# Kernel optimization log

Hardware: AMD Instinct MI355X
Metric: run time of the kernel (lower is better)

Reference implementation:

```python
import jax, jax.numpy as jnp
import numpy as np

N = 50000      # nodes
E = 800000     # edges (before self-loops)
F_IN = 768     # num_features
H = 128        # hidden_dim
C = 9          # num_classes
M = 3          # num_mid_layers
BN_EPS = 1e-5

def _glorot(k, shape):
    lim = float(np.sqrt(6.0 / (shape[-2] + shape[-1])))
    return jax.random.uniform(k, shape, jnp.float32, -lim, lim)

def setup_inputs() -> dict:
    key = jax.random.key(0)
    ks = jax.random.split(key, 24)
    x = jax.random.normal(ks[0], (N, F_IN), jnp.float32)
    edge_index = jax.random.randint(ks[1], (2, E), 0, N)
    edge_type = jax.random.randint(ks[2], (E,), 0, 5)
    edge_distance = jax.random.uniform(ks[3], (E,), jnp.float32)
    # GATConv params (heads=1): W [in,out], att_src/att_dst [out], bias [out]
    W0 = _glorot(ks[4], (F_IN, H)); a0s = _glorot(ks[5], (1, H))[0]; a0d = _glorot(ks[6], (1, H))[0]; b0 = jnp.zeros((H,), jnp.float32)
    Wm = _glorot(ks[7], (M, H, H)); ams = _glorot(ks[8], (M, 1, H))[:, 0]; amd = _glorot(ks[9], (M, 1, H))[:, 0]; bm = jnp.zeros((M, H), jnp.float32)
    W4 = _glorot(ks[10], (H, C)); a4s = _glorot(ks[11], (1, C))[0]; a4d = _glorot(ks[12], (1, C))[0]; b4 = jnp.zeros((C,), jnp.float32)
    # BatchNorm params for the M+1 norms actually used in forward (all dim H)
    gamma = jnp.ones((M + 1, H), jnp.float32)
    beta = jnp.zeros((M + 1, H), jnp.float32)
    return {"x": x, "edge_index": edge_index, "edge_type": edge_type, "edge_distance": edge_distance,
            "W0": W0, "a0s": a0s, "a0d": a0d, "b0": b0,
            "Wm": Wm, "ams": ams, "amd": amd, "bm": bm,
            "W4": W4, "a4s": a4s, "a4d": a4d, "b4": b4,
            "gamma": gamma, "beta": beta}

def _leaky(x, s):
    return jnp.where(x >= 0, x, s * x)

def _gat_conv(x, src, dst, W, a_s, a_d, b):
    # x: [N, in] -> h: [N, out]; attention per edge j->i, softmax over incoming edges of i
    h = x @ W
    alpha_src = h @ a_s            # [N]
    alpha_dst = h @ a_d            # [N]
    e = _leaky(alpha_src[src] + alpha_dst[dst], 0.2)   # [Etot]
    m = jax.ops.segment_max(e, dst, num_segments=N)
    ex = jnp.exp(e - m[dst])
    z = jax.ops.segment_sum(ex, dst, num_segments=N)
    alpha = ex / z[dst]
    out = jax.ops.segment_sum(h[src] * alpha[:, None], dst, num_segments=N)
    return out + b

def _bn_train(x, g, be):
    mu = x.mean(0)
    var = x.var(0)   # biased, as BatchNorm1d uses for normalization
    return (x - mu) * jax.lax.rsqrt(var + BN_EPS) * g + be

def reference(x, edge_index, edge_type, edge_distance,
              W0, a0s, a0d, b0, Wm, ams, amd, bm, W4, a4s, a4d, b4, gamma, beta):
    loops = jnp.arange(N, dtype=edge_index.dtype)
    src = jnp.concatenate([edge_index[0], loops])   # add self-loops (PyG default)
    dst = jnp.concatenate([edge_index[1], loops])
    h = _gat_conv(x, src, dst, W0, a0s, a0d, b0)
    for i in range(M):
        t = _leaky(_bn_train(h, gamma[i], beta[i]), 0.1)
        h = _gat_conv(t, src, dst, Wm[i], ams[i], amd[i], bm[i]) + t
    h = _leaky(_bn_train(h, gamma[M], beta[M]), 0.1)
    h = _gat_conv(h, src, dst, W4, a4s, a4d, b4)
    return _leaky(h, 0.1)
```

## Files before the change

kernel.cpp:

```cpp
#include <hip/hip_runtime.h>
#include <hip/hip_bf16.h>

#define N_NODES 50000
#define N_EDGES 800000
#define F_INN   768
#define HID     128
#define N_CLS   9
#define ETOT    (N_EDGES + N_NODES)
#define BN_EPS  1e-5f
#define INV_N   (1.0f / (float)N_NODES)

typedef __hip_bfloat16 bf16;
typedef __attribute__((ext_vector_type(8))) short bf16x8;
typedef __attribute__((ext_vector_type(4))) float f32x4;

__device__ __forceinline__ float leaky(float v, float s) { return v >= 0.0f ? v : s * v; }
__device__ __forceinline__ int clampn(int s) {
  return ((unsigned)s < (unsigned)N_NODES) ? s : 0;
}
__device__ __forceinline__ short f2bs(float f) {
  bf16 h = __float2bfloat16(f);
  return __builtin_bit_cast(short, h);
}
__device__ __forceinline__ float bs2f(unsigned short u) {
  unsigned v = ((unsigned)u) << 16;
  return __builtin_bit_cast(float, v);
}
__device__ __forceinline__ void gload_lds16(const void* g, void* l) {
  __builtin_amdgcn_global_load_lds((const __attribute__((address_space(1))) void*)g,
                                   (__attribute__((address_space(3))) void*)l, 16, 0, 0);
}

__global__ void k_pack(const float* __restrict__ W0, const float* __restrict__ Wm,
                       short* __restrict__ W0T, short* __restrict__ WmT) {
  int i = blockIdx.x * blockDim.x + threadIdx.x;
  if (i < F_INN * HID) {
    int n = i / F_INN, k = i % F_INN;
    W0T[i] = f2bs(W0[k * HID + n]);
  } else if (i < F_INN * HID + 3 * HID * HID) {
    int j = i - F_INN * HID;
    int l = j / (HID * HID), rem = j % (HID * HID);
    int n = rem / HID, k = rem % HID;
    WmT[j] = f2bs(Wm[(l * HID + k) * HID + n]);
  }
}

__global__ void k_init_deg(int* fill) {
  int i = blockIdx.x * blockDim.x + threadIdx.x;
  if (i < N_NODES) fill[i] = 1;
}

__global__ void k_count(const int* __restrict__ dst, int* fill) {
  int e = blockIdx.x * blockDim.x + threadIdx.x;
  if (e < N_EDGES) atomicAdd(&fill[clampn(dst[e])], 1);
}

__global__ void k_scan(int* fill, int* row_ptr) {
  __shared__ int wsum[16], wpre[16];
  int tid = threadIdx.x, lane = tid & 63, wv = tid >> 6;
  int carry = 0;
  for (int base = 0; base < N_NODES; base += 1024) {
    int i = base + tid;
    int v = (i < N_NODES) ? fill[i] : 0;
    if (i < N_NODES) fill[i] = 0;
    int sc = v;
#pragma unroll
    for (int off = 1; off < 64; off <<= 1) {
      int t = __shfl_up(sc, off);
      if (lane >= off) sc += t;
    }
    if (lane == 63) wsum[wv] = sc;
    __syncthreads();
    if (tid < 16) {
      int s = wsum[tid];
#pragma unroll
      for (int off = 1; off < 16; off <<= 1) {
        int t = __shfl_up(s, off);
        if (tid >= off) s += t;
      }
      wpre[tid] = s;
    }
    __syncthreads();
    int woff = wv ? wpre[wv - 1] : 0;
    if (i < N_NODES) row_ptr[i] = carry + woff + sc - v;
    carry += wpre[15];
    __syncthreads();
  }
  if (tid == 0) row_ptr[N_NODES] = carry;
}

__global__ void k_place(const int* __restrict__ src, const int* __restrict__ dst,
                        const int* __restrict__ row_ptr, int* fill, int* csr_src) {
  int id = blockIdx.x * blockDim.x + threadIdx.x;
  if (id >= ETOT) return;
  int s, d;
  if (id < N_EDGES) { s = clampn(src[id]); d = clampn(dst[id]); }
  else { s = id - N_EDGES; d = s; }
  int p = atomicAdd(&fill[d], 1);
  csr_src[row_ptr[d] + p] = s;
}

template <int K, bool BN>
__global__ __launch_bounds__(512, 5)
void k_gemm_mfma(const float* __restrict__ X, const short* __restrict__ BT,
                 const float* __restrict__ stats, const float* __restrict__ gamma,
                 const float* __restrict__ beta,
                 const float* __restrict__ a_s, const float* __restrict__ a_d,
                 short* __restrict__ hb, float* __restrict__ asrc,
                 float* __restrict__ adst) {
  constexpr int NS = K / 32;
  constexpr int SPC = 4;
  constexpr int CH = NS / SPC;
  constexpr int ROWB = K * 4;
  constexpr int XB = 16 * ROWB;
  __shared__ float4 xs4[XB / 16];
  __shared__ float psA[8][16], psD[8][16];
  __shared__ float scs[HID], sfs[HID];
  char* xs = (char*)xs4;

  int tid = threadIdx.x;
  int wid = tid >> 6, lane = tid & 63;
  int m = lane & 15, q = lane >> 4;
  int row0 = blockIdx.x * 16;
  int col0 = wid * 16;

  const short* bbase = BT + (size_t)(col0 + m) * K + q * 8;
  f32x4 acc = (f32x4){0.f, 0.f, 0.f, 0.f};
  bf16x8 bb0[SPC], bb1[SPC];

  auto loadC = [&](bf16x8* dst, int c) {
#pragma unroll
    for (int i = 0; i < SPC; ++i)
      dst[i] = *(const bf16x8*)(bbase + (size_t)(c * SPC + i) * 32);
  };
  auto computeC = [&](const bf16x8* bw, int c) {
#pragma unroll
    for (int i = 0; i < SPC; ++i) {
      int s = c * SPC + i;
      int kb = s * 128 + q * 32;
      int sw = (m & 7) << 4;
      float4 x0 = *(const float4*)(xs + m * ROWB + (kb ^ sw));
      float4 x1 = *(const float4*)(xs + m * ROWB + ((kb + 16) ^ sw));
      float xv[8] = {x0.x, x0.y, x0.z, x0.w, x1.x, x1.y, x1.z, x1.w};
      if (BN) {
        int k0 = s * 32 + q * 8;
#pragma unroll
        for (int j = 0; j < 8; ++j) xv[j] = leaky(xv[j] * scs[k0 + j] + sfs[k0 + j], 0.1f);
      }
      bf16x8 a;
#pragma unroll
      for (int j = 0; j < 8; ++j) a[j] = f2bs(xv[j]);
      acc = __builtin_amdgcn_mfma_f32_16x16x32_bf16(a, bw[i], acc, 0, 0, 0);
    }
  };

  if (BN && tid < HID) {
    float mu = stats[tid] * INV_N;
    float var = fmaxf(stats[HID + tid] * INV_N - mu * mu, 0.0f);
    float rs = rsqrtf(var + BN_EPS);
    float g = gamma[tid];
    scs[tid] = g * rs;
    sfs[tid] = beta[tid] - mu * g * rs;
  }

  loadC(bb0, 0);
  if (CH > 1) loadC(bb1, 1);
  asm volatile("" ::: "memory");
  constexpr int ROUNDS = XB / 8192;
#pragma unroll
  for (int r = 0; r < ROUNDS; ++r) {
    int o = r * 8192 + tid * 16;
    int row = o / ROWB;
    int bb = o - row * ROWB;
    int sw = (row & 7) << 4;
    gload_lds16((const char*)X + (size_t)(row0 + row) * ROWB + (bb ^ sw), xs + o);
  }
  __syncthreads();

#pragma unroll
  for (int c = 0; c < CH; ++c) {
    if (c & 1) {
      computeC(bb1, c);
      if (c + 2 < CH) { loadC(bb1, c + 2); asm volatile("" ::: "memory"); }
    } else {
      computeC(bb0, c);
      if (c + 2 < CH) { loadC(bb0, c + 2); asm volatile("" ::: "memory"); }
    }
  }

  float av = a_s[col0 + m], dv = a_d[col0 + m];
  float sr[4], dr[4];
#pragma unroll
  for (int r = 0; r < 4; ++r) {
    float cc = acc[r];
    hb[(size_t)(row0 + q * 4 + r) * HID + col0 + m] = f2bs(cc);
    sr[r] = cc * av;
    dr[r] = cc * dv;
  }
#pragma unroll
  for (int r = 0; r < 4; ++r) {
#pragma unroll
    for (int off = 1; off < 16; off <<= 1) {
      sr[r] += __shfl_xor(sr[r], off);
      dr[r] += __shfl_xor(dr[r], off);
    }
  }
  if (m == 0) {
#pragma unroll
    for (int r = 0; r < 4; ++r) {
      psA[wid][q * 4 + r] = sr[r];
      psD[wid][q * 4 + r] = dr[r];
    }
  }
  __syncthreads();
  if (tid < 16) {
    float s = 0.f, d = 0.f;
#pragma unroll
    for (int w2 = 0; w2 < 8; ++w2) { s += psA[w2][tid]; d += psD[w2][tid]; }
    asrc[row0 + tid] = s;
    adst[row0 + tid] = d;
  }
}

__device__ __forceinline__ void acc8(float* a, float e, uint4 v) {
  a[0] += e * bs2f((unsigned short)(v.x & 0xffffu));
  a[1] += e * bs2f((unsigned short)(v.x >> 16));
  a[2] += e * bs2f((unsigned short)(v.y & 0xffffu));
  a[3] += e * bs2f((unsigned short)(v.y >> 16));
  a[4] += e * bs2f((unsigned short)(v.z & 0xffffu));
  a[5] += e * bs2f((unsigned short)(v.z >> 16));
  a[6] += e * bs2f((unsigned short)(v.w & 0xffffu));
  a[7] += e * bs2f((unsigned short)(v.w >> 16));
}

__global__ void k_agg128(const unsigned short* __restrict__ h, const float* __restrict__ asrc,
                         const float* __restrict__ adst, const int* __restrict__ row_ptr,
                         const int* __restrict__ csr_src, const float* __restrict__ bias,
                         const float* __restrict__ hres, const float* __restrict__ stats,
                         const float* __restrict__ gamma, const float* __restrict__ beta,
                         float* __restrict__ out, float* __restrict__ zeroP) {
  __shared__ int   lds_ss[4][64];
  __shared__ float lds_ex[4][64];
  if (zeroP && blockIdx.x == 0 && threadIdx.x < 256) zeroP[threadIdx.x] = 0.0f;
  int wid = (blockIdx.x * blockDim.x + threadIdx.x) >> 6;
  int lane = threadIdx.x & 63;
  int w = (threadIdx.x >> 6) & 3;
  if (wid >= N_NODES) return;
  int beg = row_ptr[wid], end = row_ptr[wid + 1];
  int cnt0 = end - beg;
  float adsti = adst[wid];
  int g = lane & 15, es = lane >> 4;
  float z = 0.f;
  float a[8];
#pragma unroll
  for (int k = 0; k < 8; ++k) a[k] = 0.f;

  if (cnt0 <= 64) {
    int sl = 0;
    float v = -1e30f;
    if (lane < cnt0) {
      sl = clampn(csr_src[beg + lane]);
      v = leaky(asrc[sl] + adsti, 0.2f);
    }
    float mx = v;
#pragma unroll
    for (int off = 1; off < 64; off <<= 1) mx = fmaxf(mx, __shfl_xor(mx, off));
    float ex = (lane < cnt0) ? __expf(v - mx) : 0.f;
    lds_ss[w][lane] = sl;
    lds_ex[w][lane] = ex;
    __builtin_amdgcn_wave_barrier();
    float zs = 0.f;
    for (int jb = 0; jb < cnt0; jb += 8) {
      int j0 = jb + es, j1 = jb + 4 + es;
      int s0 = lds_ss[w][j0]; float e0 = lds_ex[w][j0];
      int s1 = lds_ss[w][j1]; float e1 = lds_ex[w][j1];
      uint4 v0 = *(const uint4*)(h + (size_t)s0 * HID + g * 8);
      uint4 v1 = *(const uint4*)(h + (size_t)s1 * HID + g * 8);
      zs += e0 + e1;
      acc8(a, e0, v0);
      acc8(a, e1, v1);
    }
    z = zs;
  } else {
    float mx = -1e30f;
    for (int cb = beg; cb < end; cb += 64) {
      int e = cb + lane;
      if (e < end) {
        int s = clampn(csr_src[e]);
        mx = fmaxf(mx, leaky(asrc[s] + adsti, 0.2f));
      }
    }
#pragma unroll
    for (int off = 1; off < 64; off <<= 1) mx = fmaxf(mx, __shfl_xor(mx, off));
    float zs = 0.f;
    for (int cb = beg; cb < end; cb += 64) {
      int cnt = min(64, end - cb);
      int sl = 0;
      float ex = 0.f;
      if (lane < cnt) {
        sl = clampn(csr_src[cb + lane]);
        ex = __expf(leaky(asrc[sl] + adsti, 0.2f) - mx);
      }
      lds_ss[w][lane] = sl;
      lds_ex[w][lane] = ex;
      __builtin_amdgcn_wave_barrier();
      for (int jb = 0; jb < cnt; jb += 8) {
        int j0 = jb + es, j1 = jb + 4 + es;
        int s0 = lds_ss[w][j0]; float e0 = lds_ex[w][j0];
        int s1 = lds_ss[w][j1]; float e1 = lds_ex[w][j1];
        uint4 v0 = *(const uint4*)(h + (size_t)s0 * HID + g * 8);
        uint4 v1 = *(const uint4*)(h + (size_t)s1 * HID + g * 8);
        zs += e0 + e1;
        acc8(a, e0, v0);
        acc8(a, e1, v1);
      }
      __builtin_amdgcn_wave_barrier();
    }
    z = zs;
  }
#pragma unroll
  for (int k = 0; k < 8; ++k) {
    a[k] += __shfl_xor(a[k], 16);
    a[k] += __shfl_xor(a[k], 32);
  }
  z += __shfl_xor(z, 16);
  z += __shfl_xor(z, 32);
  float inv = (z > 0.0f) ? 1.0f / z : 0.0f;
  if (lane < 16) {
    int c0 = g * 8;
    float o[8];
#pragma unroll
    for (int k = 0; k < 8; ++k) o[k] = a[k] * inv + bias[c0 + k];
    if (hres) {
      float hr[8];
      *(float4*)(hr)     = *(const float4*)(hres + (size_t)wid * HID + c0);
      *(float4*)(hr + 4) = *(const float4*)(hres + (size_t)wid * HID + c0 + 4);
#pragma unroll
      for (int k = 0; k < 8; ++k) {
        int c = c0 + k;
        float mu = stats[c] * INV_N;
        float var = fmaxf(stats[HID + c] * INV_N - mu * mu, 0.0f);
        float rs = rsqrtf(var + BN_EPS);
        float sc = gamma[c] * rs;
        float sf = beta[c] - mu * sc;
        o[k] += leaky(hr[k] * sc + sf, 0.1f);
      }
    }
    *(float4*)(out + (size_t)wid * HID + c0)     = *(float4*)(o);
    *(float4*)(out + (size_t)wid * HID + c0 + 4) = *(float4*)(o + 4);
  }
}

__global__ void k_bn_stats(const float* __restrict__ h, float* stats) {
  int f = threadIdx.x;
  int r0 = blockIdx.x * 128;
  int r1 = min(r0 + 128, N_NODES);
  float s = 0.0f, s2 = 0.0f;
#pragma unroll 8
  for (int r = r0; r < r1; ++r) {
    float v = h[(size_t)r * HID + f];
    s += v;
    s2 += v * v;
  }
  atomicAdd(&stats[f], s);
  atomicAdd(&stats[HID + f], s2);
}

__global__ void k_final_gemm(const float* __restrict__ h, const float* __restrict__ stats,
                             const float* __restrict__ gamma, const float* __restrict__ beta,
                             const float* __restrict__ W4,
                             const float* __restrict__ a4s, const float* __restrict__ a4d,
                             float* __restrict__ h4, float* __restrict__ asrc,
                             float* __restrict__ adst) {
  int row = (blockIdx.x * blockDim.x + threadIdx.x) >> 6;
  int lane = threadIdx.x & 63;
  if (row >= N_NODES) return;
  int c1 = lane + 64;
  float mu0 = stats[lane] * INV_N;
  float va0 = fmaxf(stats[HID + lane] * INV_N - mu0 * mu0, 0.0f);
  float rs0 = rsqrtf(va0 + BN_EPS);
  float sc0 = gamma[lane] * rs0, sf0 = beta[lane] - mu0 * sc0;
  float mu1 = stats[c1] * INV_N;
  float va1 = fmaxf(stats[HID + c1] * INV_N - mu1 * mu1, 0.0f);
  float rs1 = rsqrtf(va1 + BN_EPS);
  float sc1 = gamma[c1] * rs1, sf1 = beta[c1] - mu1 * sc1;
  float t0 = leaky(h[(size_t)row * HID + lane] * sc0 + sf0, 0.1f);
  float t1 = leaky(h[(size_t)row * HID + c1] * sc1 + sf1, 0.1f);
  float myv = 0.0f, s = 0.0f, d = 0.0f;
#pragma unroll
  for (int c = 0; c < N_CLS; ++c) {
    float p = t0 * W4[lane * N_CLS + c] + t1 * W4[(lane + 64) * N_CLS + c];
#pragma unroll
    for (int m = 32; m; m >>= 1) p += __shfl_xor(p, m);
    s += p * a4s[c];
    d += p * a4d[c];
    if (lane == c) myv = p;
  }
  if (lane < N_CLS) h4[(size_t)row * N_CLS + lane] = myv;
  if (lane == 0) { asrc[row] = s; adst[row] = d; }
}

__global__ void k_final_agg(const float* __restrict__ h4, const float* __restrict__ asrc,
                            const float* __restrict__ adst, const int* __restrict__ row_ptr,
                            const int* __restrict__ csr_src, const float* __restrict__ b4,
                            float* __restrict__ out) {
  __shared__ int   lds_ss[4][64];
  __shared__ float lds_ex[4][64];
  int wid = (blockIdx.x * blockDim.x + threadIdx.x) >> 6;
  int lane = threadIdx.x & 63;
  int w = (threadIdx.x >> 6) & 3;
  if (wid >= N_NODES) return;
  int beg = row_ptr[wid], end = row_ptr[wid + 1];
  int cnt0 = end - beg;
  float adsti = adst[wid];
  int g = lane & 15, es = lane >> 4;
  float zs = 0.f, av = 0.f;
  if (cnt0 <= 64) {
    int sl = 0;
    float v = -1e30f;
    if (lane < cnt0) {
      sl = clampn(csr_src[beg + lane]);
      v = leaky(asrc[sl] + adsti, 0.2f);
    }
    float mx = v;
#pragma unroll
    for (int off = 1; off < 64; off <<= 1) mx = fmaxf(mx, __shfl_xor(mx, off));
    float ex = (lane < cnt0) ? __expf(v - mx) : 0.f;
    lds_ss[w][lane] = sl;
    lds_ex[w][lane] = ex;
    __builtin_amdgcn_wave_barrier();
    for (int jb = 0; jb < cnt0; jb += 4) {
      int j = jb + es;
      int s = lds_ss[w][j];
      float e = lds_ex[w][j];
      zs += e;
      if (g < N_CLS) av += e * h4[(size_t)s * N_CLS + g];
    }
  } else {
    float mx = -1e30f;
    for (int cb = beg; cb < end; cb += 64) {
      int e = cb + lane;
      if (e < end) {
        int s = clampn(csr_src[e]);
        mx = fmaxf(mx, leaky(asrc[s] + adsti, 0.2f));
      }
    }
#pragma unroll
    for (int off = 1; off < 64; off <<= 1) mx = fmaxf(mx, __shfl_xor(mx, off));
    for (int cb = beg; cb < end; cb += 64) {
      int cnt = min(64, end - cb);
      int sl = 0;
      float ex = 0.f;
      if (lane < cnt) {
        sl = clampn(csr_src[cb + lane]);
        ex = __expf(leaky(asrc[sl] + adsti, 0.2f) - mx);
      }
      lds_ss[w][lane] = sl;
      lds_ex[w][lane] = ex;
      __builtin_amdgcn_wave_barrier();
      for (int jb = 0; jb < cnt; jb += 4) {
        int j = jb + es;
        int s = lds_ss[w][j];
        float e = lds_ex[w][j];
        zs += e;
        if (g < N_CLS) av += e * h4[(size_t)s * N_CLS + g];
      }
      __builtin_amdgcn_wave_barrier();
    }
  }
  float z = zs;
  z += __shfl_xor(z, 16); z += __shfl_xor(z, 32);
  av += __shfl_xor(av, 16); av += __shfl_xor(av, 32);
  if (lane < N_CLS) {
    float o = (z > 0.0f) ? av / z : 0.0f;
    o = leaky(o + b4[lane], 0.1f);
    out[(size_t)wid * N_CLS + lane] = o;
  }
}

extern "C" void kernel_launch(void* const* d_in, const int* in_sizes, int n_in,
                              void* d_out, int out_size, void* d_ws, size_t ws_size,
                              hipStream_t stream) {
  const float* x   = (const float*)d_in[0];
  const int*   ei  = (const int*)d_in[1];
  const int*   src = ei;
  const int*   dst = ei + N_EDGES;
  const float* W0  = (const float*)d_in[4];
  const float* a0s = (const float*)d_in[5];
  const float* a0d = (const float*)d_in[6];
  const float* b0  = (const float*)d_in[7];
  const float* Wm  = (const float*)d_in[8];
  const float* ams = (const float*)d_in[9];
  const float* amd = (const float*)d_in[10];
  const float* bm  = (const float*)d_in[11];
  const float* W4  = (const float*)d_in[12];
  const float* a4s = (const float*)d_in[13];
  const float* a4d = (const float*)d_in[14];
  const float* b4  = (const float*)d_in[15];
  const float* gam = (const float*)d_in[16];
  const float* bet = (const float*)d_in[17];
  float* out = (float*)d_out;

  int* row_ptr   = (int*)d_ws;
  int* fill      = row_ptr + 50004;
  int* csr_src   = fill + N_NODES;
  short* W0T     = (short*)(csr_src + ETOT);
  short* WmT     = W0T + F_INN * HID;
  short* bufA    = WmT + 3 * HID * HID;
  float* asrc    = (float*)(bufA + (size_t)N_NODES * HID);
  float* adst    = asrc + N_NODES;
  float* pstat   = adst + N_NODES;
  float* h4      = pstat + 512;
  float* bufB    = h4 + (size_t)N_NODES * N_CLS;
  float* PST[2]  = {pstat, pstat + 256};

  const int B256 = 256;
  int gN    = (N_NODES + B256 - 1) / B256;
  int gE    = (N_EDGES + B256 - 1) / B256;
  int gET   = (ETOT + B256 - 1) / B256;
  int gWav  = (N_NODES + 3) / 4;
  int gMfma = N_NODES / 16;
  int gBN   = (N_NODES + 127) / 128;
  int gPack = (F_INN * HID + 3 * HID * HID + B256 - 1) / B256;

  k_pack<<<gPack, B256, 0, stream>>>(W0, Wm, W0T, WmT);
  k_init_deg<<<gN, B256, 0, stream>>>(fill);
  k_count<<<gE, B256, 0, stream>>>(dst, fill);
  k_scan<<<1, 1024, 0, stream>>>(fill, row_ptr);
  k_place<<<gET, B256, 0, stream>>>(src, dst, row_ptr, fill, csr_src);

  k_gemm_mfma<F_INN, false><<<gMfma, 512, 0, stream>>>(x, W0T, nullptr, nullptr, nullptr,
                                                       a0s, a0d, bufA, asrc, adst);
  k_agg128<<<gWav, B256, 0, stream>>>((const unsigned short*)bufA, asrc, adst, row_ptr,
                                      csr_src, b0, nullptr, nullptr, nullptr, nullptr,
                                      bufB, PST[0]);

  for (int i = 0; i < 3; ++i) {
    k_bn_stats<<<gBN, HID, 0, stream>>>(bufB, PST[i & 1]);
    k_gemm_mfma<HID, true><<<gMfma, 512, 0, stream>>>(bufB, WmT + i * HID * HID,
                                                      PST[i & 1], gam + i * HID, bet + i * HID,
                                                      ams + i * HID, amd + i * HID,
                                                      bufA, asrc, adst);
    k_agg128<<<gWav, B256, 0, stream>>>((const unsigned short*)bufA, asrc, adst, row_ptr,
                                        csr_src, bm + i * HID, bufB, PST[i & 1],
                                        gam + i * HID, bet + i * HID, bufB, PST[(i + 1) & 1]);
  }

  k_bn_stats<<<gBN, HID, 0, stream>>>(bufB, PST[1]);
  k_final_gemm<<<gWav, B256, 0, stream>>>(bufB, PST[1], gam + 3 * HID, bet + 3 * HID,
                                          W4, a4s, a4d, h4, asrc, adst);
  k_final_agg<<<gWav, B256, 0, stream>>>(h4, asrc, adst, row_ptr, csr_src, b4, out);
}
```

Measured before the change: 808.0 us.

## Make MFMA GEMM persistent with register-resident weights and double-buffered LDS staging

Measured after the change: 775.4 us. -4.0%, faster.

```diff
diff --git a/kernel.cpp b/kernel.cpp
--- a/kernel.cpp
+++ b/kernel.cpp
@@ -9,6 +9,7 @@
 #define ETOT    (N_EDGES + N_NODES)
 #define BN_EPS  1e-5f
 #define INV_N   (1.0f / (float)N_NODES)
+#define NT16    (N_NODES / 16)
 
 typedef __hip_bfloat16 bf16;
 typedef __attribute__((ext_vector_type(8))) short bf16x8;
@@ -29,6 +30,14 @@
 __device__ __forceinline__ void gload_lds16(const void* g, void* l) {
   __builtin_amdgcn_global_load_lds((const __attribute__((address_space(1))) void*)g,
                                    (__attribute__((address_space(3))) void*)l, 16, 0, 0);
+}
+__device__ __forceinline__ void blk_barrier() {
+  asm volatile("" ::: "memory");
+  __builtin_amdgcn_s_barrier();
+  __builtin_amdgcn_sched_barrier(0);
+}
+__device__ __forceinline__ void lgkm0() {
+  asm volatile("s_waitcnt lgkmcnt(0)" ::: "memory");
 }
 
 __global__ void k_pack(const float* __restrict__ W0, const float* __restrict__ Wm,
@@ -101,124 +110,148 @@
 }
 
 template <int K, bool BN>
-__global__ __launch_bounds__(512, 5)
+__global__ __launch_bounds__(512, 2)
 void k_gemm_mfma(const float* __restrict__ X, const short* __restrict__ BT,
                  const float* __restrict__ stats, const float* __restrict__ gamma,
                  const float* __restrict__ beta,
                  const float* __restrict__ a_s, const float* __restrict__ a_d,
                  short* __restrict__ hb, float* __restrict__ asrc,
                  float* __restrict__ adst) {
-  constexpr int NS = K / 32;
-  constexpr int SPC = 4;
-  constexpr int CH = NS / SPC;
-  constexpr int ROWB = K * 4;
-  constexpr int XB = 16 * ROWB;
-  __shared__ float4 xs4[XB / 16];
+  constexpr int KSUB  = (K > 384) ? 384 : K;
+  constexpr int NSUB  = K / KSUB;
+  constexpr int NS    = KSUB / 32;
+  constexpr int LPT   = KSUB / 128;
+  constexpr int NSLOT = KSUB * 2;
+  __shared__ float4 bufF[2][KSUB * 4];
+  __shared__ bf16x8 bufH[NSLOT];
+  __shared__ float scs[HID], sfs[HID];
   __shared__ float psA[8][16], psD[8][16];
-  __shared__ float scs[HID], sfs[HID];
-  char* xs = (char*)xs4;
-
-  int tid = threadIdx.x;
-  int wid = tid >> 6, lane = tid & 63;
-  int m = lane & 15, q = lane >> 4;
-  int row0 = blockIdx.x * 16;
-  int col0 = wid * 16;
-
-  const short* bbase = BT + (size_t)(col0 + m) * K + q * 8;
-  f32x4 acc = (f32x4){0.f, 0.f, 0.f, 0.f};
-  bf16x8 bb0[SPC], bb1[SPC];
-
-  auto loadC = [&](bf16x8* dst, int c) {
-#pragma unroll
-    for (int i = 0; i < SPC; ++i)
-      dst[i] = *(const bf16x8*)(bbase + (size_t)(c * SPC + i) * 32);
-  };
-  auto computeC = [&](const bf16x8* bw, int c) {
-#pragma unroll
-    for (int i = 0; i < SPC; ++i) {
-      int s = c * SPC + i;
-      int kb = s * 128 + q * 32;
-      int sw = (m & 7) << 4;
-      float4 x0 = *(const float4*)(xs + m * ROWB + (kb ^ sw));
-      float4 x1 = *(const float4*)(xs + m * ROWB + ((kb + 16) ^ sw));
-      float xv[8] = {x0.x, x0.y, x0.z, x0.w, x1.x, x1.y, x1.z, x1.w};
-      if (BN) {
-        int k0 = s * 32 + q * 8;
-#pragma unroll
-        for (int j = 0; j < 8; ++j) xv[j] = leaky(xv[j] * scs[k0 + j] + sfs[k0 + j], 0.1f);
-      }
-      bf16x8 a;
-#pragma unroll
-      for (int j = 0; j < 8; ++j) a[j] = f2bs(xv[j]);
-      acc = __builtin_amdgcn_mfma_f32_16x16x32_bf16(a, bw[i], acc, 0, 0, 0);
-    }
-  };
+
+  const int tid = threadIdx.x;
+  const int wv = tid >> 6, lane = tid & 63;
+  const int m = lane & 15, q = lane >> 4;
+  const int col = wv * 16 + m;
+  const int bid = blockIdx.x;
+  const int nrt = (NT16 - bid + 255) >> 8;
+  const int T = nrt * NSUB;
+
+  bf16x8 breg[K / 32];
+  {
+    const short* bb = BT + (size_t)col * K + q * 8;
+#pragma unroll
+    for (int c = 0; c < K / 32; ++c) breg[c] = *(const bf16x8*)(bb + c * 32);
+  }
+  const float av = a_s[col], dv = a_d[col];
 
   if (BN && tid < HID) {
     float mu = stats[tid] * INV_N;
     float var = fmaxf(stats[HID + tid] * INV_N - mu * mu, 0.0f);
     float rs = rsqrtf(var + BN_EPS);
-    float g = gamma[tid];
-    scs[tid] = g * rs;
-    sfs[tid] = beta[tid] - mu * g * rs;
-  }
-
-  loadC(bb0, 0);
-  if (CH > 1) loadC(bb1, 1);
-  asm volatile("" ::: "memory");
-  constexpr int ROUNDS = XB / 8192;
-#pragma unroll
-  for (int r = 0; r < ROUNDS; ++r) {
-    int o = r * 8192 + tid * 16;
-    int row = o / ROWB;
-    int bb = o - row * ROWB;
-    int sw = (row & 7) << 4;
-    gload_lds16((const char*)X + (size_t)(row0 + row) * ROWB + (bb ^ sw), xs + o);
-  }
-  __syncthreads();
-
-#pragma unroll
-  for (int c = 0; c < CH; ++c) {
-    if (c & 1) {
-      computeC(bb1, c);
-      if (c + 2 < CH) { loadC(bb1, c + 2); asm volatile("" ::: "memory"); }
+    float g2 = gamma[tid];
+    scs[tid] = g2 * rs;
+    sfs[tid] = beta[tid] - mu * g2 * rs;
+  }
+
+  auto STAGE = [&](int t) {
+    int r0 = (bid + (t / NSUB) * 256) * 16;
+    int kb = (NSUB == 2) ? (t & 1) * KSUB : 0;
+    int buf = t & 1;
+#pragma unroll
+    for (int r = 0; r < LPT; ++r) {
+      int d = r * 512 + tid;
+      int row = d & 15, c = d >> 4;
+      gload_lds16(X + (size_t)(r0 + row) * K + kb + c * 4, &bufF[buf][d]);
+    }
+  };
+
+  STAGE(0);
+  if (T > 1) STAGE(1);
+  lgkm0();
+  blk_barrier();
+
+  f32x4 acc = (f32x4){0.f, 0.f, 0.f, 0.f};
+  for (int t = 0; t < T; ++t) {
+    const int ks = (NSUB == 2) ? (t & 1) : 0;
+    const int buf = t & 1;
+    if (t + 1 < T) {
+      if constexpr (LPT == 3) asm volatile("s_waitcnt vmcnt(3)" ::: "memory");
+      else                    asm volatile("s_waitcnt vmcnt(1)" ::: "memory");
     } else {
-      computeC(bb0, c);
-      if (c + 2 < CH) { loadC(bb0, c + 2); asm volatile("" ::: "memory"); }
-    }
-  }
-
-  float av = a_s[col0 + m], dv = a_d[col0 + m];
-  float sr[4], dr[4];
-#pragma unroll
-  for (int r = 0; r < 4; ++r) {
-    float cc = acc[r];
-    hb[(size_t)(row0 + q * 4 + r) * HID + col0 + m] = f2bs(cc);
-    sr[r] = cc * av;
-    dr[r] = cc * dv;
-  }
-#pragma unroll
-  for (int r = 0; r < 4; ++r) {
-#pragma unroll
-    for (int off = 1; off < 16; off <<= 1) {
-      sr[r] += __shfl_xor(sr[r], off);
-      dr[r] += __shfl_xor(dr[r], off);
-    }
-  }
-  if (m == 0) {
-#pragma unroll
-    for (int r = 0; r < 4; ++r) {
-      psA[wid][q * 4 + r] = sr[r];
-      psD[wid][q * 4 + r] = dr[r];
-    }
-  }
-  __syncthreads();
-  if (tid < 16) {
-    float s = 0.f, d = 0.f;
-#pragma unroll
-    for (int w2 = 0; w2 < 8; ++w2) { s += psA[w2][tid]; d += psD[w2][tid]; }
-    asrc[row0 + tid] = s;
-    adst[row0 + tid] = d;
+      asm volatile("s_waitcnt vmcnt(0)" ::: "memory");
+    }
+    blk_barrier();
+#pragma unroll
+    for (int j = 0; j < (NSLOT + 511) / 512; ++j) {
+      int sl = j * 512 + tid;
+      if (sl < NSLOT) {
+        int s = sl >> 6, lp = sl & 63;
+        int mp = lp & 15, qp = lp >> 4;
+        int k0 = s * 32 + qp * 8;
+        int d = (k0 >> 2) * 16 + mp;
+        float4 x0 = bufF[buf][d];
+        float4 x1 = bufF[buf][d + 16];
+        float xv[8] = {x0.x, x0.y, x0.z, x0.w, x1.x, x1.y, x1.z, x1.w};
+        if (BN) {
+#pragma unroll
+          for (int jj = 0; jj < 8; ++jj)
+            xv[jj] = leaky(xv[jj] * scs[k0 + jj] + sfs[k0 + jj], 0.1f);
+        }
+        bf16x8 hv;
+#pragma unroll
+        for (int jj = 0; jj < 8; ++jj) hv[jj] = f2bs(xv[jj]);
+        bufH[sl] = hv;
+      }
+    }
+    lgkm0();
+    blk_barrier();
+    if (t + 2 < T) STAGE(t + 2);
+    if (NSUB == 2 && ks == 1) {
+#pragma unroll
+      for (int s = 0; s < NS; ++s)
+        acc = __builtin_amdgcn_mfma_f32_16x16x32_bf16(bufH[s * 64 + lane],
+                                                      breg[NS + s], acc, 0, 0, 0);
+    } else {
+#pragma unroll
+      for (int s = 0; s < NS; ++s)
+        acc = __builtin_amdgcn_mfma_f32_16x16x32_bf16(bufH[s * 64 + lane],
+                                                      breg[s], acc, 0, 0, 0);
+    }
+    if (ks == NSUB - 1) {
+      int r0 = (bid + (t / NSUB) * 256) * 16;
+      float sr[4], dr[4];
+#pragma unroll
+      for (int r = 0; r < 4; ++r) {
+        float cc = acc[r];
+        hb[(size_t)(r0 + q * 4 + r) * HID + col] = f2bs(cc);
+        sr[r] = cc * av;
+        dr[r] = cc * dv;
+      }
+      acc = (f32x4){0.f, 0.f, 0.f, 0.f};
+#pragma unroll
+      for (int r = 0; r < 4; ++r) {
+#pragma unroll
+        for (int off = 1; off < 16; off <<= 1) {
+          sr[r] += __shfl_xor(sr[r], off);
+          dr[r] += __shfl_xor(dr[r], off);
+        }
+      }
+      if (m == 0) {
+#pragma unroll
+        for (int r = 0; r < 4; ++r) {
+          psA[wv][q * 4 + r] = sr[r];
+          psD[wv][q * 4 + r] = dr[r];
+        }
+      }
+      lgkm0();
+      blk_barrier();
+      if (tid < 16) {
+        float s2 = 0.f, d2 = 0.f;
+#pragma unroll
+        for (int w2 = 0; w2 < 8; ++w2) { s2 += psA[w2][tid]; d2 += psD[w2][tid]; }
+        asrc[r0 + tid] = s2;
+        adst[r0 + tid] = d2;
+      }
+    }
   }
 }
 
@@ -269,17 +302,26 @@
     lds_ss[w][lane] = sl;
     lds_ex[w][lane] = ex;
     __builtin_amdgcn_wave_barrier();
+    int nr = (cnt0 + 7) >> 3;
+    int s0 = lds_ss[w][es],     s1 = lds_ss[w][es + 4];
+    float e0 = lds_ex[w][es],   e1 = lds_ex[w][es + 4];
+    uint4 v0 = *(const uint4*)(h + (size_t)s0 * HID + g * 8);
+    uint4 v1 = *(const uint4*)(h + (size_t)s1 * HID + g * 8);
     float zs = 0.f;
-    for (int jb = 0; jb < cnt0; jb += 8) {
-      int j0 = jb + es, j1 = jb + 4 + es;
-      int s0 = lds_ss[w][j0]; float e0 = lds_ex[w][j0];
-      int s1 = lds_ss[w][j1]; float e1 = lds_ex[w][j1];
-      uint4 v0 = *(const uint4*)(h + (size_t)s0 * HID + g * 8);
-      uint4 v1 = *(const uint4*)(h + (size_t)s1 * HID + g * 8);
+    for (int r = 1; r < nr; ++r) {
+      int j0 = r * 8 + es, j1 = r * 8 + 4 + es;
+      int t0 = lds_ss[w][j0];   float f0 = lds_ex[w][j0];
+      int t1 = lds_ss[w][j1];   float f1 = lds_ex[w][j1];
+      uint4 n0 = *(const uint4*)(h + (size_t)t0 * HID + g * 8);
+      uint4 n1 = *(const uint4*)(h + (size_t)t1 * HID + g * 8);
       zs += e0 + e1;
       acc8(a, e0, v0);
       acc8(a, e1, v1);
-    }
+      v0 = n0; v1 = n1; e0 = f0; e1 = f1;
+    }
+    zs += e0 + e1;
+    acc8(a, e0, v0);
+    acc8(a, e1, v1);
     z = zs;
   } else {
     float mx = -1e30f;
@@ -429,13 +471,21 @@
     lds_ss[w][lane] = sl;
     lds_ex[w][lane] = ex;
     __builtin_amdgcn_wave_barrier();
-    for (int jb = 0; jb < cnt0; jb += 4) {
-      int j = jb + es;
-      int s = lds_ss[w][j];
-      float e = lds_ex[w][j];
-      zs += e;
-      if (g < N_CLS) av += e * h4[(size_t)s * N_CLS + g];
-    }
+    int nr = (cnt0 + 3) >> 2;
+    int s0 = lds_ss[w][es];
+    float e0 = lds_ex[w][es];
+    float hv0 = (g < N_CLS) ? h4[(size_t)s0 * N_CLS + g] : 0.f;
+    for (int r = 1; r < nr; ++r) {
+      int j = r * 4 + es;
+      int s1 = lds_ss[w][j];
+      float e1 = lds_ex[w][j];
+      float hv1 = (g < N_CLS) ? h4[(size_t)s1 * N_CLS + g] : 0.f;
+      zs += e0;
+      av += e0 * hv0;
+      s0 = s1; e0 = e1; hv0 = hv1;
+    }
+    zs += e0;
+    av += e0 * hv0;
   } else {
     float mx = -1e30f;
     for (int cb = beg; cb < end; cb += 64) {
@@ -519,7 +569,6 @@
   int gE    = (N_EDGES + B256 - 1) / B256;
   int gET   = (ETOT + B256 - 1) / B256;
   int gWav  = (N_NODES + 3) / 4;
-  int gMfma = N_NODES / 16;
   int gBN   = (N_NODES + 127) / 128;
   int gPack = (F_INN * HID + 3 * HID * HID + B256 - 1) / B256;
 
@@ -529,18 +578,18 @@
   k_scan<<<1, 1024, 0, stream>>>(fill, row_ptr);
   k_place<<<gET, B256, 0, stream>>>(src, dst, row_ptr, fill, csr_src);
 
-  k_gemm_mfma<F_INN, false><<<gMfma, 512, 0, stream>>>(x, W0T, nullptr, nullptr, nullptr,
-                                                       a0s, a0d, bufA, asrc, adst);
+  k_gemm_mfma<F_INN, false><<<256, 512, 0, stream>>>(x, W0T, nullptr, nullptr, nullptr,
+                                                     a0s, a0d, bufA, asrc, adst);
   k_agg128<<<gWav, B256, 0, stream>>>((const unsigned short*)bufA, asrc, adst, row_ptr,
                                       csr_src, b0, nullptr, nullptr, nullptr, nullptr,
                                       bufB, PST[0]);
 
   for (int i = 0; i < 3; ++i) {
     k_bn_stats<<<gBN, HID, 0, stream>>>(bufB, PST[i & 1]);
-    k_gemm_mfma<HID, true><<<gMfma, 512, 0, stream>>>(bufB, WmT + i * HID * HID,
-                                                      PST[i & 1], gam + i * HID, bet + i * HID,
-                                                      ams + i * HID, amd + i * HID,
-                                                      bufA, asrc, adst);
+    k_gemm_mfma<HID, true><<<256, 512, 0, stream>>>(bufB, WmT + i * HID * HID,
+                                                    PST[i & 1], gam + i * HID, bet + i * HID,
+                                                    ams + i * HID, amd + i * HID,
+                                                    bufA, asrc, adst);
     k_agg128<<<gWav, B256, 0, stream>>>((const unsigned short*)bufA, asrc, adst, row_ptr,
                                         csr_src, bm + i * HID, bufB, PST[i & 1],
                                         gam + i * HID, bet + i * HID, bufB, PST[(i + 1) & 1]);
```
